# Optimization experiments

Measured on AMD Instinct MI355X. Metric: run time of the kernel, lower is better.

## Reference

```python
import jax, jax.numpy as jnp
import numpy as np
from jax import lax

J = 3  # number of decomposition levels
SQ2 = float(1.0 / np.sqrt(2.0))


def _corr(Xp, hr, axis, Lout, stride):
    """Strided valid correlation of padded Xp with taps hr along `axis`.
    out[n] = sum_k hr[k] * Xp[n*stride + k]. Tap loop is over <=10 static taps."""
    m = hr.shape[0]
    hi = stride * (Lout - 1) + 1
    acc = hr[0] * lax.slice_in_dim(Xp, 0, hi, stride, axis)
    for k in range(1, m):
        acc = acc + hr[k] * lax.slice_in_dim(Xp, k, k + hi, stride, axis)
    return acc


def colfilter(X, h):
    # 'same' convolution along H with symmetric (edge-repeat) extension.
    m = h.shape[0]; m2 = m // 2; L = X.shape[2]
    Xp = jnp.pad(X, ((0, 0), (0, 0), (m2, m2), (0, 0)), mode='symmetric')
    return _corr(Xp, h[::-1], 2, L, 1)  # corr with reversed taps == convolution


def rowfilter(X, h):
    m = h.shape[0]; m2 = m // 2; L = X.shape[3]
    Xp = jnp.pad(X, ((0, 0), (0, 0), (0, 0), (m2, m2)), mode='symmetric')
    return _corr(Xp, h[::-1], 3, L, 1)


def coldfilt(X, ha, hb, highpass):
    # Dual-tree decimated (by 2) filtering along H. r must be a multiple of 4.
    b, c, r, w = X.shape
    m = ha.shape[0]; r4 = r // 4
    Xp = jnp.pad(X, ((0, 0), (0, 0), (m, m), (0, 0)), mode='symmetric')
    E = Xp[:, :, 2::2, :]  # even-phase stream, len r/2+m-1
    O = Xp[:, :, 3::2, :]  # odd-phase stream
    a_out = _corr(O, ha[::-1], 2, r4, 2)
    b_out = _corr(E, hb[::-1], 2, r4, 2)
    ev, od = (b_out, a_out) if highpass else (a_out, b_out)
    return jnp.stack([ev, od], axis=3).reshape(b, c, r // 2, w)


def rowdfilt(X, ha, hb, highpass):
    b, c, r, w = X.shape
    m = ha.shape[0]; w4 = w // 4
    Xp = jnp.pad(X, ((0, 0), (0, 0), (0, 0), (m, m)), mode='symmetric')
    E = Xp[:, :, :, 2::2]
    O = Xp[:, :, :, 3::2]
    a_out = _corr(O, ha[::-1], 3, w4, 2)
    b_out = _corr(E, hb[::-1], 3, w4, 2)
    ev, od = (b_out, a_out) if highpass else (a_out, b_out)
    return jnp.stack([ev, od], axis=4).reshape(b, c, r, w // 2)


def q2c(y):
    # Convert quads of real pixels into two complex subbands.
    y = y * SQ2
    a = y[..., 0::2, 0::2]; b = y[..., 0::2, 1::2]
    c = y[..., 1::2, 0::2]; d = y[..., 1::2, 1::2]
    return (a - d, b + c), (a + d, b - c)


def _bands(lh, hh, hl):
    # Orientation order [15, 45, 75, 105, 135, 165] deg; real/imag in last dim.
    (r15, i15), (r165, i165) = q2c(lh)
    (r45, i45), (r135, i135) = q2c(hh)
    (r75, i75), (r105, i105) = q2c(hl)
    c = lambda re, im: jnp.stack([re, im], axis=-1)
    return jnp.stack([c(r15, i15), c(r45, i45), c(r75, i75),
                      c(r105, i105), c(r135, i135), c(r165, i165)], axis=2)


def dtcwt_forward(x, h0o, h1o, h0a, h0b, h1a, h1b):
    # Level 1 (undecimated biorthogonal filters; q2c decimates bandpass by 2).
    lo = rowfilter(x, h0o)
    hi = rowfilter(x, h1o)
    ll = colfilter(lo, h0o)
    yh = [_bands(colfilter(lo, h1o), colfilter(hi, h1o), colfilter(hi, h0o))]
    # Levels 2..J (quarter-shift dual-tree decimated filters).
    for _ in range(1, J):
        lo = rowdfilt(ll, h0b, h0a, False)
        hi = rowdfilt(ll, h1b, h1a, True)
        lh = coldfilt(lo, h1b, h1a, True)
        hl = coldfilt(hi, h0b, h0a, False)
        hh = coldfilt(hi, h1b, h1a, True)
        ll = coldfilt(lo, h0b, h0a, False)
        yh.append(_bands(lh, hh, hl))
    return (ll, yh[0], yh[1], yh[2])


def _filters():
    h0o = np.array([-0.05, 0.25, 0.6, 0.25, -0.05], dtype=np.float32)
    h1o = np.array([-3/280, 3/56, 73/280, -17/28, 73/280, 3/56, -3/280],
                   dtype=np.float32)
    h0a = np.array([0.03516384, 0.0, -0.08832942, 0.23389032, 0.76027237,
                    0.58751830, 0.0, -0.11430184, 0.0, 0.0], dtype=np.float32)
    h0b = h0a[::-1].copy()
    alt = ((-1.0) ** np.arange(10)).astype(np.float32)
    h1a = h0b * alt
    h1b = h1a[::-1].copy()
    return {k: jnp.asarray(v) for k, v in dict(
        h0o=h0o, h1o=h1o, h0a=h0a, h0b=h0b, h1a=h1a, h1b=h1b).items()}


def setup_inputs() -> dict:
    key = jax.random.key(0)
    x = jax.random.normal(key, (8, 16, 256, 256), dtype=jnp.float32)
    inp = {'x': x}
    inp.update(_filters())
    return inp


def reference(x, h0o, h1o, h0a, h0b, h1a, h1b):
    return dtcwt_forward(x, h0o, h1o, h0a, h0b, h1a, h1b)
```

## Files before the change

kernel.cpp:

```cpp
#include <hip/hip_runtime.h>

#define SQ2F 0.70710678118654752440f

static constexpr float H0O[5] = {-0.05f, 0.25f, 0.6f, 0.25f, -0.05f};
static constexpr float H1O[7] = {(float)(-3.0/280.0), (float)(3.0/56.0), (float)(73.0/280.0),
                                 (float)(-17.0/28.0), (float)(73.0/280.0), (float)(3.0/56.0),
                                 (float)(-3.0/280.0)};
static constexpr float H0A[10] = {0.03516384f, 0.0f, -0.08832942f, 0.23389032f, 0.76027237f,
                                  0.5875183f, 0.0f, -0.11430184f, 0.0f, 0.0f};
static constexpr float H0B[10] = {0.0f, 0.0f, -0.11430184f, 0.0f, 0.5875183f,
                                  0.76027237f, 0.23389032f, -0.08832942f, 0.0f, 0.03516384f};
static constexpr float H1A[10] = {0.0f, 0.0f, -0.11430184f, 0.0f, 0.5875183f,
                                  -0.76027237f, 0.23389032f, 0.08832942f, 0.0f, -0.03516384f};
static constexpr float H1B[10] = {-0.03516384f, 0.0f, 0.08832942f, 0.23389032f, -0.76027237f,
                                  0.5875183f, 0.0f, -0.11430184f, 0.0f, 0.0f};

__device__ __forceinline__ int symref(int t, int L) {
    if (t < 0) t = -1 - t;
    if (t >= L) t = 2 * L - 1 - t;
    return t;
}

__device__ __forceinline__ void gload_lds16(const float* g, float* lds) {
    __builtin_amdgcn_global_load_lds(
        (const __attribute__((address_space(1))) void*)g,
        (__attribute__((address_space(3))) void*)lds, 16, 0, 0);
}

__device__ __forceinline__ float2 f2add(float2 a, float2 b) { return make_float2(a.x + b.x, a.y + b.y); }
__device__ __forceinline__ float2 f2fma(float s, float2 a, float2 b) {
    return make_float2(fmaf(s, a.x, b.x), fmaf(s, a.y, b.y));
}
__device__ __forceinline__ float2 f2s(float s, float2 a) { return make_float2(s * a.x, s * a.y); }

__device__ __forceinline__ float2 f2sym7(float2 a, float2 b, float2 c, float2 d,
                                         float2 e, float2 f, float2 g) {
    float2 r = f2s(H1O[3], d);
    r = f2fma(H1O[0], f2add(a, g), r);
    r = f2fma(H1O[1], f2add(b, f), r);
    r = f2fma(H1O[2], f2add(c, e), r);
    return r;
}
__device__ __forceinline__ float2 f2sym5(float2 a, float2 b, float2 c, float2 d, float2 e) {
    float2 r = f2s(H0O[2], c);
    r = f2fma(H0O[0], f2add(a, e), r);
    r = f2fma(H0O[1], f2add(b, d), r);
    return r;
}
__device__ __forceinline__ float4 f4sym5(float4 a, float4 b, float4 c, float4 d, float4 e) {
    float4 r;
    r.x = fmaf(H0O[0], a.x + e.x, fmaf(H0O[1], b.x + d.x, H0O[2] * c.x));
    r.y = fmaf(H0O[0], a.y + e.y, fmaf(H0O[1], b.y + d.y, H0O[2] * c.y));
    r.z = fmaf(H0O[0], a.z + e.z, fmaf(H0O[1], b.z + d.z, H0O[2] * c.z));
    r.w = fmaf(H0O[0], a.w + e.w, fmaf(H0O[1], b.w + d.w, H0O[2] * c.w));
    return r;
}

#define XS(r,c)  S[(r)*92 + (c)]
#define LS(r,c)  S[(r)*84 + (c)]
#define LOS(r,c) S[4784 + (r)*84 + (c)]
#define LO2(r,c) S[4784 + (r)*34 + (c)]
#define HI2(r,c) S[6416 + (r)*34 + (c)]
#define HIS(r,c) S[9152 + (r)*68 + (c)]

__global__ __launch_bounds__(512, 6) void dtcwt_l12(
    const float* __restrict__ x,
    float* __restrict__ yh0,
    float* __restrict__ yh1,
    float* __restrict__ ll2)
{
    __shared__ __align__(16) float S[11736];
    int tid = threadIdx.x, bx = blockIdx.x;
    int tj = bx & 3, ti = (bx >> 2) & 7, bc = bx >> 5;
    const int xr0 = 32 * ti - 10, xc0 = 64 * tj - 12;
    const float* xb = x + (size_t)bc * 65536;
    const int lane = tid & 63;

    for (int u = tid; u < 1196; u += 512) {
        int r = u / 23, q = u - 23 * r;
        int rr = symref(xr0 + r, 256);
        int g  = xc0 + 4 * q;
        g = (g < 0) ? 0 : ((g > 252) ? 252 : g);
        gload_lds16(xb + (size_t)rr * 256 + g, &S[4 * (u - lane)]);
    }
    __syncthreads();

    if (tj == 0) {
        for (int p = tid; p < 624; p += 512) {
            int r = p / 12, c = p - 12 * r;
            S[r * 92 + c] = S[r * 92 + (23 - c)];
        }
        __syncthreads();
    } else if (tj == 3) {
        for (int p = tid; p < 832; p += 512) {
            int r = p >> 4, c = 76 + (p & 15);
            S[r * 92 + c] = S[r * 92 + (151 - c)];
        }
        __syncthreads();
    }

    for (int p = tid; p < 520; p += 512) {
        int r = p / 10, s = p - r * 10, c8 = 8 * s;
        const float* xr = &XS(r, c8);
        float4 q0 = *(const float4*)&xr[0];
        float4 q1 = *(const float4*)&xr[4];
        float4 q2 = *(const float4*)&xr[8];
        float4 q3 = *(const float4*)&xr[12];
        float u[16] = {q0.x,q0.y,q0.z,q0.w, q1.x,q1.y,q1.z,q1.w,
                       q2.x,q2.y,q2.z,q2.w, q3.x,q3.y,q3.z,q3.w};
        float l[8];
        #pragma unroll
        for (int j = 0; j < 8; j++)
            l[j] = fmaf(H0O[0], u[j+2] + u[j+6],
                   fmaf(H0O[1], u[j+3] + u[j+5], H0O[2] * u[j+4]));
        *(float4*)&LOS(r, c8)     = make_float4(l[0], l[1], l[2], l[3]);
        *(float4*)&LOS(r, c8 + 4) = make_float4(l[4], l[5], l[6], l[7]);
    }
    for (int p = tid; p < 304; p += 512) {
        int r = p >> 3, s = p & 7, c8 = 8 * s;
        const float* xr = &XS(r + 7, c8 + 8);
        float4 q0 = *(const float4*)&xr[0];
        float4 q1 = *(const float4*)&xr[4];
        float4 q2 = *(const float4*)&xr[8];
        float4 q3 = *(const float4*)&xr[12];
        float w[16] = {q0.x,q0.y,q0.z,q0.w, q1.x,q1.y,q1.z,q1.w,
                       q2.x,q2.y,q2.z,q2.w, q3.x,q3.y,q3.z,q3.w};
        float h[8];
        #pragma unroll
        for (int j = 0; j < 8; j++)
            h[j] = fmaf(H1O[0], w[j+1] + w[j+7],
                   fmaf(H1O[1], w[j+2] + w[j+6],
                   fmaf(H1O[2], w[j+3] + w[j+5], H1O[3] * w[j+4])));
        *(float4*)&HIS(r, c8)     = make_float4(h[0], h[1], h[2], h[3]);
        *(float4*)&HIS(r, c8 + 4) = make_float4(h[4], h[5], h[6], h[7]);
    }
    __syncthreads();

    for (int p = tid; p < 480; p += 512) {
        int rp = p / 20, s = p - rp * 20, c4 = 4 * s;
        const float* l0 = &LOS(2 * rp, c4);
        float4 m0 = *(const float4*)&l0[0];
        float4 m1 = *(const float4*)&l0[84];
        float4 m2 = *(const float4*)&l0[168];
        float4 m3 = *(const float4*)&l0[252];
        float4 m4 = *(const float4*)&l0[336];
        float4 m5 = *(const float4*)&l0[420];
        *(float4*)&LS(2 * rp,     c4) = f4sym5(m0, m1, m2, m3, m4);
        *(float4*)&LS(2 * rp + 1, c4) = f4sym5(m1, m2, m3, m4, m5);
    }
    {
        float* yb = yh0 + (size_t)bc * 196608;
        const size_t bs = 32768;
        int cp = tid & 31, oi = tid >> 5;
        float2 low[8], hiw[8];
        #pragma unroll
        for (int k = 0; k < 8; k++) {
            low[k] = *(const float2*)&LOS(2 * oi + 7 + k, 2 * cp + 8);
            hiw[k] = *(const float2*)&HIS(2 * oi + k,     2 * cp);
        }
        float2 lhe = f2s(SQ2F, f2sym7(low[0],low[1],low[2],low[3],low[4],low[5],low[6]));
        float2 lho = f2s(SQ2F, f2sym7(low[1],low[2],low[3],low[4],low[5],low[6],low[7]));
        float2 hhe = f2s(SQ2F, f2sym7(hiw[0],hiw[1],hiw[2],hiw[3],hiw[4],hiw[5],hiw[6]));
        float2 hho = f2s(SQ2F, f2sym7(hiw[1],hiw[2],hiw[3],hiw[4],hiw[5],hiw[6],hiw[7]));
        float2 hle = f2s(SQ2F, f2sym5(hiw[1],hiw[2],hiw[3],hiw[4],hiw[5]));
        float2 hlo = f2s(SQ2F, f2sym5(hiw[2],hiw[3],hiw[4],hiw[5],hiw[6]));
        int i0 = 16 * ti + oi, j0 = 32 * tj + cp;
        size_t pix = ((size_t)i0 * 128 + j0) * 2;
        { float a=lhe.x, b=lhe.y, c=lho.x, d=lho.y;
          *(float2*)&yb[0*bs + pix] = make_float2(a-d, b+c);
          *(float2*)&yb[5*bs + pix] = make_float2(a+d, b-c); }
        { float a=hhe.x, b=hhe.y, c=hho.x, d=hho.y;
          *(float2*)&yb[1*bs + pix] = make_float2(a-d, b+c);
          *(float2*)&yb[4*bs + pix] = make_float2(a+d, b-c); }
        { float a=hle.x, b=hle.y, c=hlo.x, d=hlo.y;
          *(float2*)&yb[2*bs + pix] = make_float2(a-d, b+c);
          *(float2*)&yb[3*bs + pix] = make_float2(a+d, b-c); }
    }
    __syncthreads();

    for (int p = tid; p < 768; p += 512) {
        int nl = p / 48, r = p - nl * 48;
        const float* lsr = &LS(r, 4 * nl);
        float4 q0 = *(const float4*)&lsr[0];
        float4 q1 = *(const float4*)&lsr[4];
        float4 q2 = *(const float4*)&lsr[8];
        float4 q3 = *(const float4*)&lsr[12];
        float4 q4 = *(const float4*)&lsr[16];
        float v[20] = {q0.x,q0.y,q0.z,q0.w, q1.x,q1.y,q1.z,q1.w, q2.x,q2.y,q2.z,q2.w,
                       q3.x,q3.y,q3.z,q3.w, q4.x,q4.y,q4.z,q4.w};
        float aLo = 0.f, bLo = 0.f, aHi = 0.f, bHi = 0.f;
        #pragma unroll
        for (int t = 0; t < 10; t++) {
            float vo = v[19 - 2*t], ve = v[18 - 2*t];
            aLo = fmaf(H0B[t], vo, aLo); bLo = fmaf(H0A[t], ve, bLo);
            aHi = fmaf(H1B[t], vo, aHi); bHi = fmaf(H1A[t], ve, bHi);
        }
        *(float2*)&LO2(r, 2*nl) = make_float2(aLo, bLo);
        *(float2*)&HI2(r, 2*nl) = make_float2(bHi, aHi);
    }
    __syncthreads();

    if (tid < 256) {
        int half = tid >> 7, q = tid & 127;
        int cp = q & 15, li = q >> 4;
        int i1 = 8 * ti + li;
        const float* Bp = half ? &HI2(0, 0) : &LO2(0, 0);
        float2 v[20];
        #pragma unroll
        for (int k = 0; k < 20; k++)
            v[k] = *(const float2*)&Bp[(4 * li + k) * 34 + 2 * cp];
        float2 z = make_float2(0.f, 0.f);
        float2 aA = z, bA = z, aB = z, bB = z;
        #pragma unroll
        for (int t = 0; t < 10; t++) {
            float2 vo = v[19 - 2*t], ve = v[18 - 2*t];
            aA = f2fma(H0B[t], vo, aA); bA = f2fma(H0A[t], ve, bA);
            aB = f2fma(H1B[t], vo, aB); bB = f2fma(H1A[t], ve, bB);
        }
        float* yb = yh1 + (size_t)bc * 49152;
        int j1 = 16 * tj + cp;
        size_t pix = ((size_t)i1 * 64 + j1) * 2;
        const size_t bs = 8192;
        if (half == 0) {
            float* llb = ll2 + (size_t)bc * 16384;
            int gc = 32 * tj + 2 * cp;
            *(float2*)&llb[(size_t)(2*i1)     * 128 + gc] = aA;
            *(float2*)&llb[(size_t)(2*i1 + 1) * 128 + gc] = bA;
            float a = SQ2F*bB.x, b = SQ2F*bB.y, c = SQ2F*aB.x, d = SQ2F*aB.y;
            *(float2*)&yb[0*bs + pix] = make_float2(a-d, b+c);
            *(float2*)&yb[5*bs + pix] = make_float2(a+d, b-c);
        } else {
            float a = SQ2F*bB.x, b = SQ2F*bB.y, c = SQ2F*aB.x, d = SQ2F*aB.y;
            *(float2*)&yb[1*bs + pix] = make_float2(a-d, b+c);
            *(float2*)&yb[4*bs + pix] = make_float2(a+d, b-c);
            a = SQ2F*aA.x; b = SQ2F*aA.y; c = SQ2F*bA.x; d = SQ2F*bA.y;
            *(float2*)&yb[2*bs + pix] = make_float2(a-d, b+c);
            *(float2*)&yb[3*bs + pix] = make_float2(a+d, b-c);
        }
    }
}

#define X2(r,c)  S2[(r)*84 + (c)]
#define LO3(r,c) S2[6720 + (r)*34 + (c)]
#define HI3(r,c) S2[9440 + (r)*34 + (c)]

__global__ __launch_bounds__(512) void level_fused(
    const float* __restrict__ X,
    float* __restrict__ llout,
    float* __restrict__ yh,
    int R, int C, int nbi, int nbj)
{
    __shared__ __align__(16) float S2[12160];

    int tid = threadIdx.x;
    int bx  = blockIdx.x;
    int tj = bx % nbj; int ti = (bx / nbj) % nbi; int bc = bx / (nbj * nbi);
    int i0 = ti * 16, j0 = tj * 16;
    int gr0 = 4 * i0 - 8, gc0 = 4 * j0 - 8;
    const float* Xb = X + (size_t)bc * R * C;
    const int lane = tid & 63;

    for (int u = tid; u < 1680; u += 512) {
        int r = u / 21, q = u - 21 * r;
        int rr = symref(gr0 + r, R);
        int g  = gc0 + 4 * q;
        g = (g < 0) ? 0 : ((g > C - 4) ? (C - 4) : g);
        gload_lds16(Xb + (size_t)rr * C + g, &S2[4 * (u - lane)]);
    }
    __syncthreads();

    int cl = (gc0 < 0) ? -gc0 : 0;
    int cr = (gc0 + 80 > C) ? (C - gc0) : 80;
    if (cl > 0) {
        for (int p = tid; p < 640; p += 512) {
            int r = p >> 3, c = p & 7;
            X2(r, c) = X2(r, (-1 - 2 * gc0) - c);
        }
    }
    if (cr < 80) {
        for (int p = tid; p < 640; p += 512) {
            int r = p >> 3, c = cr + (p & 7);
            X2(r, c) = X2(r, (2 * C - 1 - 2 * gc0) - c);
        }
    }
    if (cl > 0 || cr < 80) __syncthreads();

    for (int p = tid; p < 1280; p += 512) {
        int nl = p / 80, r = p - nl * 80;
        const float* xr = &X2(r, 4 * nl);
        float4 q0 = *(const float4*)&xr[0];
        float4 q1 = *(const float4*)&xr[4];
        float4 q2 = *(const float4*)&xr[8];
        float4 q3 = *(const float4*)&xr[12];
        float4 q4 = *(const float4*)&xr[16];
        float v[20] = {q0.x,q0.y,q0.z,q0.w, q1.x,q1.y,q1.z,q1.w, q2.x,q2.y,q2.z,q2.w,
                       q3.x,q3.y,q3.z,q3.w, q4.x,q4.y,q4.z,q4.w};
        float aLo = 0.f, bLo = 0.f, aHi = 0.f, bHi = 0.f;
        #pragma unroll
        for (int t = 0; t < 10; t++) {
            float vo = v[19 - 2*t], ve = v[18 - 2*t];
            aLo = fmaf(H0B[t], vo, aLo); bLo = fmaf(H0A[t], ve, bLo);
            aHi = fmaf(H1B[t], vo, aHi); bHi = fmaf(H1A[t], ve, bHi);
        }
        *(float2*)&LO3(r, 2 * nl) = make_float2(aLo, bLo);
        *(float2*)&HI3(r, 2 * nl) = make_float2(bHi, aHi);
    }
    __syncthreads();

    {
        int half = tid >> 8, q8 = tid & 255;
        int lj = q8 & 15, li = q8 >> 4;
        int i = i0 + li, j = j0 + lj;
        const float* Bp = half ? &HI3(0, 0) : &LO3(0, 0);
        float2 v[20];
        #pragma unroll
        for (int k = 0; k < 20; k++)
            v[k] = *(const float2*)&Bp[(4 * li + k) * 34 + 2 * lj];
        float2 z = make_float2(0.f, 0.f);
        float2 aA = z, bA = z, aB = z, bB = z;
        #pragma unroll
        for (int t = 0; t < 10; t++) {
            float2 vo = v[19 - 2*t], ve = v[18 - 2*t];
            aA = f2fma(H0B[t], vo, aA); bA = f2fma(H0A[t], ve, bA);
            aB = f2fma(H1B[t], vo, aB); bB = f2fma(H1A[t], ve, bB);
        }
        int R4 = R >> 2, Wq = C >> 2, C2 = C >> 1;
        float* yb = yh + (size_t)bc * 6 * R4 * Wq * 2;
        size_t pix = ((size_t)i * Wq + j) * 2;
        size_t bs  = (size_t)R4 * Wq * 2;
        if (half == 0) {
            float* llb = llout + (size_t)bc * (R >> 1) * C2;
            *(float2*)&llb[(size_t)(2*i)   * C2 + 2*j] = aA;
            *(float2*)&llb[(size_t)(2*i+1) * C2 + 2*j] = bA;
            float a = SQ2F*bB.x, b = SQ2F*bB.y, c = SQ2F*aB.x, d = SQ2F*aB.y;
            *(float2*)&yb[0*bs + pix] = make_float2(a-d, b+c);
            *(float2*)&yb[5*bs + pix] = make_float2(a+d, b-c);
        } else {
            float a = SQ2F*bB.x, b = SQ2F*bB.y, c = SQ2F*aB.x, d = SQ2F*aB.y;
            *(float2*)&yb[1*bs + pix] = make_float2(a-d, b+c);
            *(float2*)&yb[4*bs + pix] = make_float2(a+d, b-c);
            a = SQ2F*aA.x; b = SQ2F*aA.y; c = SQ2F*bA.x; d = SQ2F*bA.y;
            *(float2*)&yb[2*bs + pix] = make_float2(a-d, b+c);
            *(float2*)&yb[3*bs + pix] = make_float2(a+d, b-c);
        }
    }
}

extern "C" void kernel_launch(void* const* d_in, const int* in_sizes, int n_in,
                              void* d_out, int out_size, void* d_ws, size_t ws_size,
                              hipStream_t stream) {
    const float* x = (const float*)d_in[0];
    float* out = (float*)d_out;

    const int BC = 8 * 16;

    float* out_ll  = out;
    float* out_yh0 = out + 524288;
    float* out_yh1 = out + 25690112;
    float* out_yh2 = out + 31981568;

    float* ll2 = (float*)d_ws;

    dtcwt_l12<<<BC * 32, 512, 0, stream>>>(x, out_yh0, out_yh1, ll2);

    level_fused<<<BC * 4, 512, 0, stream>>>(ll2, out_ll, out_yh2, 128, 128, 2, 2);
}
```

Before: 182.0 us.

## Remap block order and load halo edges directly from global memory

Both kernels remap blockIdx, interleaving by 8 (likely for XCD/L2 locality across adjacent tiles). Edge tiles no longer load clamped data and then mirror it in LDS behind a second barrier. Interior columns now arrive through per-row async global->LDS loads, and the reflected halo columns are read straight from global memory, so only one __syncthreads remains. The level kernel's staged width changes from 80 to 84 columns to match the row stride. This adds scalar global loads on edge tiles and relies on the block-count assumptions baked into the swizzle.

```diff
diff --git a/kernel.cpp b/kernel.cpp
--- a/kernel.cpp
+++ b/kernel.cpp
@@ -70,34 +70,45 @@
     float* __restrict__ ll2)
 {
     __shared__ __align__(16) float S[11736];
-    int tid = threadIdx.x, bx = blockIdx.x;
+    int tid = threadIdx.x;
+    int bx0 = blockIdx.x;
+    int bx  = ((bx0 & 7) << 9) | (bx0 >> 3);
     int tj = bx & 3, ti = (bx >> 2) & 7, bc = bx >> 5;
     const int xr0 = 32 * ti - 10, xc0 = 64 * tj - 12;
     const float* xb = x + (size_t)bc * 65536;
     const int lane = tid & 63;
-
-    for (int u = tid; u < 1196; u += 512) {
-        int r = u / 23, q = u - 23 * r;
-        int rr = symref(xr0 + r, 256);
-        int g  = xc0 + 4 * q;
-        g = (g < 0) ? 0 : ((g > 252) ? 252 : g);
-        gload_lds16(xb + (size_t)rr * 256 + g, &S[4 * (u - lane)]);
-    }
-    __syncthreads();
-
-    if (tj == 0) {
+    const int wv = tid >> 6;
+
+    if (tj == 1 || tj == 2) {
+        for (int u = tid; u < 1196; u += 512) {
+            int r = u / 23, q = u - 23 * r;
+            int rr = symref(xr0 + r, 256);
+            gload_lds16(xb + (size_t)rr * 256 + (xc0 + 4 * q), &S[4 * (u - lane)]);
+        }
+    } else if (tj == 0) {
+        for (int r = wv; r < 52; r += 8) {
+            int rr = symref(xr0 + r, 256);
+            if (lane < 20)
+                gload_lds16(xb + (size_t)rr * 256 + 4 * lane, &S[r * 92 + 12]);
+        }
         for (int p = tid; p < 624; p += 512) {
             int r = p / 12, c = p - 12 * r;
-            S[r * 92 + c] = S[r * 92 + (23 - c)];
-        }
-        __syncthreads();
-    } else if (tj == 3) {
+            int rr = symref(xr0 + r, 256);
+            S[r * 92 + c] = xb[(size_t)rr * 256 + (11 - c)];
+        }
+    } else {
+        for (int r = wv; r < 52; r += 8) {
+            int rr = symref(xr0 + r, 256);
+            if (lane < 19)
+                gload_lds16(xb + (size_t)rr * 256 + 180 + 4 * lane, &S[r * 92]);
+        }
         for (int p = tid; p < 832; p += 512) {
             int r = p >> 4, c = 76 + (p & 15);
-            S[r * 92 + c] = S[r * 92 + (151 - c)];
-        }
-        __syncthreads();
-    }
+            int rr = symref(xr0 + r, 256);
+            S[r * 92 + c] = xb[(size_t)rr * 256 + (331 - c)];
+        }
+    }
+    __syncthreads();
 
     for (int p = tid; p < 520; p += 512) {
         int r = p / 10, s = p - r * 10, c8 = 8 * s;
@@ -253,37 +264,39 @@
     __shared__ __align__(16) float S2[12160];
 
     int tid = threadIdx.x;
-    int bx  = blockIdx.x;
+    int bx0 = blockIdx.x;
+    int bx  = ((bx0 & 7) << 6) | (bx0 >> 3);
     int tj = bx % nbj; int ti = (bx / nbj) % nbi; int bc = bx / (nbj * nbi);
     int i0 = ti * 16, j0 = tj * 16;
     int gr0 = 4 * i0 - 8, gc0 = 4 * j0 - 8;
     const float* Xb = X + (size_t)bc * R * C;
     const int lane = tid & 63;
-
-    for (int u = tid; u < 1680; u += 512) {
-        int r = u / 21, q = u - 21 * r;
+    const int wv = tid >> 6;
+
+    int cl = (gc0 < 0) ? -gc0 : 0;
+    int cr = (gc0 + 84 > C) ? (C - gc0) : 84;
+    int nu = (cr - cl) >> 2;
+    for (int r = wv; r < 80; r += 8) {
         int rr = symref(gr0 + r, R);
-        int g  = gc0 + 4 * q;
-        g = (g < 0) ? 0 : ((g > C - 4) ? (C - 4) : g);
-        gload_lds16(Xb + (size_t)rr * C + g, &S2[4 * (u - lane)]);
-    }
-    __syncthreads();
-
-    int cl = (gc0 < 0) ? -gc0 : 0;
-    int cr = (gc0 + 80 > C) ? (C - gc0) : 80;
+        if (lane < nu)
+            gload_lds16(Xb + (size_t)rr * C + (gc0 + cl) + 4 * lane,
+                        &S2[r * 84 + cl]);
+    }
     if (cl > 0) {
         for (int p = tid; p < 640; p += 512) {
             int r = p >> 3, c = p & 7;
-            X2(r, c) = X2(r, (-1 - 2 * gc0) - c);
-        }
-    }
-    if (cr < 80) {
-        for (int p = tid; p < 640; p += 512) {
-            int r = p >> 3, c = cr + (p & 7);
-            X2(r, c) = X2(r, (2 * C - 1 - 2 * gc0) - c);
-        }
-    }
-    if (cl > 0 || cr < 80) __syncthreads();
+            int rr = symref(gr0 + r, R);
+            S2[r * 84 + c] = Xb[(size_t)rr * C + (-1 - gc0 - c)];
+        }
+    }
+    if (cr < 84) {
+        for (int p = tid; p < 960; p += 512) {
+            int r = p / 12, c = cr + (p - r * 12);
+            int rr = symref(gr0 + r, R);
+            S2[r * 84 + c] = Xb[(size_t)rr * C + (2 * C - 1 - gc0 - c)];
+        }
+    }
+    __syncthreads();
 
     for (int p = tid; p < 1280; p += 512) {
         int nl = p / 80, r = p - nl * 80;
```

Result: slower. 189.5 us (+4.1%).
